# Optimization experiments

Hardware: AMD Instinct MI355X
Metric: run time of the kernel (lower is better)

The kernel has to match this reference:

```python
import jax, jax.numpy as jnp
import numpy as np

EPS = 1e-5      # BatchNorm eps
SLOPE = 0.2     # LeakyReLU negative slope
K = 20          # hardcoded k in Net
OUT_CH = 64     # AGConv out_channels
IN_CH = 6       # AGConv in_channels (= 2*3)


def _bn(x, gamma, beta, axis):
    # Inference-mode BatchNorm: running_mean=0, running_var=1
    shape = [1] * x.ndim
    shape[axis] = -1
    scale = (gamma / jnp.sqrt(1.0 + EPS)).reshape(shape)
    return x * scale + beta.reshape(shape)


def _lrelu(x):
    return jnp.where(x >= 0, x, SLOPE * x)


def _graph_feature(x, k):
    # x: (B, C, N) -> feature (B, 2C, N, k) as in get_graph_feature
    B, C, N = x.shape
    xt = jnp.swapaxes(x, 1, 2)                        # (B, N, C)
    inner = -2.0 * jnp.einsum('bci,bcj->bij', x, x)   # (B, N, N)
    xx = jnp.sum(x * x, axis=1)                       # (B, N)
    pd = -xx[:, :, None] - inner - xx[:, None, :]     # -||xi-xj||^2
    idx = jax.lax.top_k(pd, k)[1]                     # (B, N, k) nearest neighbors
    b_idx = jnp.arange(B)[:, None, None]
    nbr = xt[b_idx, idx]                              # (B, N, k, C) gather
    center = jnp.broadcast_to(xt[:, :, None, :], nbr.shape)
    feat = jnp.concatenate([nbr - center, center], axis=-1)  # (B, N, k, 2C)
    return jnp.moveaxis(feat, -1, 1)                  # (B, 2C, N, k)


def setup_inputs() -> dict:
    key = jax.random.key(0)
    ks = jax.random.split(key, 5)
    B, N = 4, 4096
    x = jax.random.normal(ks[0], (B, 3, N), dtype=jnp.float32)
    w0 = jax.random.normal(ks[1], (OUT_CH, IN_CH), dtype=jnp.float32) * 0.2
    w1 = jax.random.normal(ks[2], (OUT_CH * IN_CH, OUT_CH), dtype=jnp.float32) * 0.05
    w_out = jax.random.normal(ks[3], (3, OUT_CH), dtype=jnp.float32) * 0.1
    return {
        'x': x,
        'w0': w0, 'g0': jnp.ones(OUT_CH), 'b0': jnp.zeros(OUT_CH),
        'w1': w1, 'g1': jnp.ones(OUT_CH), 'b1': jnp.zeros(OUT_CH),
        'w_out': w_out, 'g_out': jnp.ones(3), 'b_out': jnp.zeros(3),
    }


def reference(x, w0, g0, b0, w1, g1, b1, w_out, g_out, b_out):
    # x: (B, 3, N). feat == both `x` and `p` in the torch code (points is x,
    # same idx), so compute once.
    feat = _graph_feature(x, K)                       # (B, 6, N, k)
    B, _, N, k = feat.shape
    # AGConv: weight-generating branch
    y = jnp.einsum('oc,bcnk->bonk', w0, feat)         # conv0 1x1
    y = _lrelu(_bn(y, g0, b0, 1))
    y = jnp.einsum('oc,bcnk->bonk', w1, y)            # conv1 1x1 -> (B, 384, N, k)
    y = jnp.moveaxis(y, 1, -1).reshape(B, N, k, OUT_CH, IN_CH)
    xg = jnp.moveaxis(feat, 1, -1)                    # (B, N, k, 6)
    z = jnp.einsum('bnkoc,bnkc->bnko', y, xg)         # per-edge dynamic matmul
    z = jnp.moveaxis(z, -1, 1)                        # (B, 64, N, k)
    z = _lrelu(_bn(z, g1, b1, 1))
    x1 = jnp.max(z, axis=-1)                          # max over neighbors -> (B, 64, N)
    out = jnp.einsum('oc,bcn->bon', w_out, x1)        # Net.conv1 1x1
    out = _lrelu(_bn(out, g_out, b_out, 1))
    return out
```

## Files before the change

kernel.cpp:

```cpp
#include <hip/hip_runtime.h>
#include <hip/hip_bf16.h>

#define NPTS 4096
#define BATCH 4
#define KNN 20

typedef __attribute__((ext_vector_type(8))) short bf16x8;
typedef __attribute__((ext_vector_type(4))) float f32x4;
typedef __attribute__((ext_vector_type(4))) int i32x4;
typedef unsigned long long u64;

#define OFF_W0S   0
#define OFF_B0F   384
#define OFF_S1F   448
#define OFF_B1F   512
#define OFF_WOUTS 576
#define OFF_BOUTF 768
#define OFF_WHI_BYTES 4096
#define OFF_WLO_BYTES 53248
#define OFF_IDX_BYTES 102400
#define OFF_XQ_BYTES  757760

__device__ __forceinline__ u64 shflx64(u64 v, int off) {
  int lo = __shfl_xor((int)(v & 0xFFFFFFFFull), off);
  int hi = __shfl_xor((int)(v >> 32), off);
  return ((u64)(unsigned)hi << 32) | (unsigned)lo;
}
__device__ __forceinline__ u64 shflbc64(u64 v, int src) {
  int lo = __shfl((int)(v & 0xFFFFFFFFull), src);
  int hi = __shfl((int)(v >> 32), src);
  return ((u64)(unsigned)hi << 32) | (unsigned)lo;
}

__global__ __launch_bounds__(256) void prep_kernel(
    const float* __restrict__ x,
    const float* __restrict__ w0, const float* __restrict__ g0, const float* __restrict__ b0,
    const float* __restrict__ w1, const float* __restrict__ g1, const float* __restrict__ b1,
    const float* __restrict__ wout, const float* __restrict__ gout, const float* __restrict__ bout,
    float* __restrict__ wsf, unsigned short* __restrict__ whi, unsigned short* __restrict__ wlo,
    float4* __restrict__ xq) {
  const float rs = 1.0f / sqrtf(1.0f + 1e-5f);
  int t = blockIdx.x * 256 + threadIdx.x;
  if (t < 384) wsf[OFF_W0S + t] = w0[t] * (g0[t / 6] * rs);
  if (t < 64) {
    wsf[OFF_B0F + t] = b0[t];
    wsf[OFF_S1F + t] = g1[t] * rs;
    wsf[OFF_B1F + t] = b1[t];
  }
  if (t < 192) wsf[OFF_WOUTS + t] = wout[t] * (gout[t / 64] * rs);
  if (t < 3) wsf[OFF_BOUTF + t] = bout[t];
  if (t < BATCH * NPTS) {
    int bb = t >> 12, j = t & (NPTS - 1);
    const float* xb = x + bb * 3 * NPTS;
    float x0 = xb[j], x1 = xb[NPTS + j], x2 = xb[2 * NPTS + j];
    float xx = x0 * x0 + x1 * x1 + x2 * x2;
    xq[t] = make_float4(x0, x1, x2, xx);
  }
  if (t < 24576) {
    int j = t & 7, L = (t >> 3) & 63, ft = t >> 9;
    int kk = ft >> 2, nt = ft & 3;
    int k = kk * 32 + ((L >> 4) << 3) + j;
    int c = k >> 6, d = k & 63;
    int o = nt * 16 + (L & 15);
    float w = w1[(o * 6 + c) * 64 + d];
    unsigned bw = __float_as_uint(w);
    unsigned hb = bw & 0xFFFF0000u;
    float r = w - __uint_as_float(hb);
    whi[t] = (unsigned short)(bw >> 16);
    wlo[t] = (unsigned short)(__float_as_uint(r) >> 16);
  }
}

__global__ __launch_bounds__(64, 4) void knn_kernel(const float4* __restrict__ xq,
                                                    unsigned short* __restrict__ idxbuf) {
  const int pt = blockIdx.x;
  const int b = pt >> 12, n = pt & (NPTS - 1);
  const int lane = threadIdx.x;
  const float4* xqb = xq + b * NPTS;
  const float4 xin = xqb[n];
  const float xi0 = xin.x, xi1 = xin.y, xi2 = xin.z;
  const float nxxi = -xin.w;

  u64 k1 = 0, k2 = 0;
  unsigned lo = 4095u - (unsigned)lane;
#pragma unroll 4
  for (int s = 0; s < 64; ++s) {
    float4 q = xqb[s * 64 + lane];
    float dot = xi0 * q.x + xi1 * q.y + xi2 * q.z;
    float inner = -2.0f * dot;
    float pd = (nxxi - inner) - q.w;
    u64 k = ((u64)(~__float_as_uint(pd)) << 32) | lo;
    lo -= 64u;
    bool c1 = k > k1;
    bool c2 = k > k2;
    u64 t = c1 ? k1 : k;
    k2 = c2 ? t : k2;
    k1 = c1 ? k : k1;
  }

  u64 tk = 0;
  unsigned myout = 0;
#pragma unroll 1
  for (int r = 0; r < KNN; ++r) {
    u64 bk = k1;
    for (int off = 32; off > 0; off >>= 1) {
      u64 ok = shflx64(bk, off);
      if (ok > bk) bk = ok;
    }
    unsigned bj = 4095u - (unsigned)(bk & 4095u);
    if (lane == r) myout = bj;
    bool owner = (k1 == bk);
    u64 bit = 1ull << (bj >> 6);
    if (owner) {
      tk |= bit;
      k1 = k2;
      k2 = 0;
    }
    bool need = owner && (k1 == 0);
    u64 nm = __ballot(need);
    if (nm) {
      int LN = __ffsll(nm) - 1;
      int j2 = lane * 64 + LN;
      float4 q = xqb[j2];
      float dot = xi0 * q.x + xi1 * q.y + xi2 * q.z;
      float inner = -2.0f * dot;
      float pd = (nxxi - inner) - q.w;
      u64 kk = ((u64)(~__float_as_uint(pd)) << 32) | (4095u - (unsigned)j2);
      u64 tkl = shflbc64(tk, LN);
      if ((tkl >> lane) & 1) kk = 0;
      u64 w1k = kk;
      for (int off = 32; off > 0; off >>= 1) {
        u64 ok = shflx64(w1k, off);
        if (ok > w1k) w1k = ok;
      }
      u64 kk2 = (kk == w1k) ? 0 : kk;
      u64 w2k = kk2;
      for (int off = 32; off > 0; off >>= 1) {
        u64 ok = shflx64(w2k, off);
        if (ok > w2k) w2k = ok;
      }
      if (lane == LN) { k1 = w1k; k2 = w2k; }
    }
  }
  if (lane < KNN) idxbuf[pt * KNN + lane] = (unsigned short)myout;
}

__global__ __launch_bounds__(64, 2) void mlp_kernel(const float4* __restrict__ xq,
                                                    const float* __restrict__ wsf,
                                                    const unsigned short* __restrict__ whi,
                                                    const unsigned short* __restrict__ wlo,
                                                    const unsigned short* __restrict__ idxbuf,
                                                    float* __restrict__ out) {
  __shared__ float w0l[448];
  __shared__ float v6l[80 * 12];
  __shared__ float pmax[20 * 66];

  const int lane = threadIdx.x;
  const int quad = lane >> 4, l15 = lane & 15;
  const int pt_base = blockIdx.x * 4;

  for (int i = lane; i < 448; i += 64) w0l[i] = wsf[i];

#pragma unroll
  for (int rep = 0; rep < 2; ++rep) {
    int e = rep * 64 + lane;
    if (e < 80) {
      int p = e / 20, el = e - p * 20;
      int pt = pt_base + p;
      int b = pt >> 12, n = pt & (NPTS - 1);
      float4 xi = xq[b * NPTS + n];
      int jn = idxbuf[pt * KNN + el];
      float4 xj = xq[b * NPTS + jn];
      v6l[e * 12 + 0] = xj.x - xi.x;
      v6l[e * 12 + 1] = xj.y - xi.y;
      v6l[e * 12 + 2] = xj.z - xi.z;
      v6l[e * 12 + 3] = xi.x;
      v6l[e * 12 + 4] = xi.y;
      v6l[e * 12 + 5] = xi.z;
    }
  }
  __syncthreads();

  float v6r[5][6];
#pragma unroll
  for (int t = 0; t < 5; ++t) {
    const float* vr = v6l + (t * 16 + l15) * 12;
    f32x4 a4 = *(const f32x4*)vr;
    v6r[t][0] = a4.x; v6r[t][1] = a4.y; v6r[t][2] = a4.z; v6r[t][3] = a4.w;
    v6r[t][4] = vr[4]; v6r[t][5] = vr[5];
  }
  float hf[5][2][8];
#pragma unroll
  for (int hh = 0; hh < 2; ++hh) {
#pragma unroll
    for (int j = 0; j < 8; ++j) {
      const int d = hh * 32 + quad * 8 + j;
      const float* wr = w0l + d * 6;
      float wc0 = wr[0], wc1 = wr[1], wc2 = wr[2];
      float wc3 = wr[3], wc4 = wr[4], wc5 = wr[5];
      float bb = w0l[384 + d];
#pragma unroll
      for (int t = 0; t < 5; ++t) {
        float a = bb + wc0 * v6r[t][0] + wc1 * v6r[t][1] + wc2 * v6r[t][2]
                     + wc3 * v6r[t][3] + wc4 * v6r[t][4] + wc5 * v6r[t][5];
        hf[t][hh][j] = fmaxf(a, 0.2f * a);
      }
    }
  }

  f32x4 acc[5][4];
#pragma unroll
  for (int t = 0; t < 5; ++t)
#pragma unroll
    for (int nt = 0; nt < 4; ++nt) acc[t][nt] = (f32x4){0.f, 0.f, 0.f, 0.f};

  const i32x4* whp = (const i32x4*)whi;
  const i32x4* wlp = (const i32x4*)wlo;

#pragma unroll
  for (int kk = 0; kk < 12; ++kk) {
    const int c = kk >> 1, hh = kk & 1;
    i32x4 wh[4], wl[4];
#pragma unroll
    for (int nt = 0; nt < 4; ++nt) {
      wh[nt] = whp[(kk * 4 + nt) * 64 + lane];
      wl[nt] = wlp[(kk * 4 + nt) * 64 + lane];
    }
#pragma unroll
    for (int t = 0; t < 5; ++t) {
      float vc = v6l[(t * 16 + l15) * 12 + c];
      float u0 = vc * hf[t][hh][0], u1 = vc * hf[t][hh][1];
      float u2 = vc * hf[t][hh][2], u3 = vc * hf[t][hh][3];
      float u4 = vc * hf[t][hh][4], u5 = vc * hf[t][hh][5];
      float u6 = vc * hf[t][hh][6], u7 = vc * hf[t][hh][7];
      unsigned ub0 = __float_as_uint(u0), ub1 = __float_as_uint(u1);
      unsigned ub2 = __float_as_uint(u2), ub3 = __float_as_uint(u3);
      unsigned ub4 = __float_as_uint(u4), ub5 = __float_as_uint(u5);
      unsigned ub6 = __float_as_uint(u6), ub7 = __float_as_uint(u7);
      float r0 = u0 - __uint_as_float(ub0 & 0xFFFF0000u);
      float r1 = u1 - __uint_as_float(ub1 & 0xFFFF0000u);
      float r2 = u2 - __uint_as_float(ub2 & 0xFFFF0000u);
      float r3 = u3 - __uint_as_float(ub3 & 0xFFFF0000u);
      float r4 = u4 - __uint_as_float(ub4 & 0xFFFF0000u);
      float r5 = u5 - __uint_as_float(ub5 & 0xFFFF0000u);
      float r6 = u6 - __uint_as_float(ub6 & 0xFFFF0000u);
      float r7 = u7 - __uint_as_float(ub7 & 0xFFFF0000u);
      i32x4 ah, al;
      ah.x = __builtin_amdgcn_perm(ub1, ub0, 0x07060302);
      ah.y = __builtin_amdgcn_perm(ub3, ub2, 0x07060302);
      ah.z = __builtin_amdgcn_perm(ub5, ub4, 0x07060302);
      ah.w = __builtin_amdgcn_perm(ub7, ub6, 0x07060302);
      al.x = __builtin_amdgcn_perm(__float_as_uint(r1), __float_as_uint(r0), 0x07060302);
      al.y = __builtin_amdgcn_perm(__float_as_uint(r3), __float_as_uint(r2), 0x07060302);
      al.z = __builtin_amdgcn_perm(__float_as_uint(r5), __float_as_uint(r4), 0x07060302);
      al.w = __builtin_amdgcn_perm(__float_as_uint(r7), __float_as_uint(r6), 0x07060302);
      bf16x8 ahv = __builtin_bit_cast(bf16x8, ah);
      bf16x8 alv = __builtin_bit_cast(bf16x8, al);
#pragma unroll
      for (int nt = 0; nt < 4; ++nt) {
        bf16x8 bh = __builtin_bit_cast(bf16x8, wh[nt]);
        bf16x8 bl = __builtin_bit_cast(bf16x8, wl[nt]);
        acc[t][nt] = __builtin_amdgcn_mfma_f32_16x16x32_bf16(ahv, bh, acc[t][nt], 0, 0, 0);
        acc[t][nt] = __builtin_amdgcn_mfma_f32_16x16x32_bf16(ahv, bl, acc[t][nt], 0, 0, 0);
        acc[t][nt] = __builtin_amdgcn_mfma_f32_16x16x32_bf16(alv, bh, acc[t][nt], 0, 0, 0);
      }
    }
  }
  __syncthreads();

  float s1v[4], b1v[4];
#pragma unroll
  for (int nt = 0; nt < 4; ++nt) {
    s1v[nt] = wsf[OFF_S1F + nt * 16 + l15];
    b1v[nt] = wsf[OFF_B1F + nt * 16 + l15];
  }
#pragma unroll
  for (int t = 0; t < 5; ++t) {
#pragma unroll
    for (int nt = 0; nt < 4; ++nt) {
      f32x4 a = acc[t][nt];
      float z0 = a.x * s1v[nt] + b1v[nt]; z0 = fmaxf(z0, 0.2f * z0);
      float z1 = a.y * s1v[nt] + b1v[nt]; z1 = fmaxf(z1, 0.2f * z1);
      float z2 = a.z * s1v[nt] + b1v[nt]; z2 = fmaxf(z2, 0.2f * z2);
      float z3 = a.w * s1v[nt] + b1v[nt]; z3 = fmaxf(z3, 0.2f * z3);
      float m4 = fmaxf(fmaxf(z0, z1), fmaxf(z2, z3));
      pmax[(t * 4 + quad) * 66 + nt * 16 + l15] = m4;
    }
  }
  __syncthreads();

  float woutr[3];
#pragma unroll
  for (int m = 0; m < 3; ++m) woutr[m] = wsf[OFF_WOUTS + m * 64 + lane];
#pragma unroll
  for (int p = 0; p < 4; ++p) {
    float x1 = pmax[(p * 5 + 0) * 66 + lane];
    x1 = fmaxf(x1, pmax[(p * 5 + 1) * 66 + lane]);
    x1 = fmaxf(x1, pmax[(p * 5 + 2) * 66 + lane]);
    x1 = fmaxf(x1, pmax[(p * 5 + 3) * 66 + lane]);
    x1 = fmaxf(x1, pmax[(p * 5 + 4) * 66 + lane]);
    int pt = pt_base + p;
    int b = pt >> 12, n = pt & (NPTS - 1);
#pragma unroll
    for (int m = 0; m < 3; ++m) {
      float part = woutr[m] * x1;
      for (int off = 32; off > 0; off >>= 1) part += __shfl_xor(part, off);
      if (lane == 0) {
        float ov = part + wsf[OFF_BOUTF + m];
        out[(b * 3 + m) * NPTS + n] = fmaxf(ov, 0.2f * ov);
      }
    }
  }
}

extern "C" void kernel_launch(void* const* d_in, const int* in_sizes, int n_in,
                              void* d_out, int out_size, void* d_ws, size_t ws_size,
                              hipStream_t stream) {
  const float* x    = (const float*)d_in[0];
  const float* w0   = (const float*)d_in[1];
  const float* g0   = (const float*)d_in[2];
  const float* b0   = (const float*)d_in[3];
  const float* w1   = (const float*)d_in[4];
  const float* g1   = (const float*)d_in[5];
  const float* b1   = (const float*)d_in[6];
  const float* wout = (const float*)d_in[7];
  const float* gout = (const float*)d_in[8];
  const float* bout = (const float*)d_in[9];
  float* wsf = (float*)d_ws;
  unsigned short* whi = (unsigned short*)((char*)d_ws + OFF_WHI_BYTES);
  unsigned short* wlo = (unsigned short*)((char*)d_ws + OFF_WLO_BYTES);
  unsigned short* idxbuf = (unsigned short*)((char*)d_ws + OFF_IDX_BYTES);
  float4* xq = (float4*)((char*)d_ws + OFF_XQ_BYTES);
  float* out = (float*)d_out;

  prep_kernel<<<96, 256, 0, stream>>>(x, w0, g0, b0, w1, g1, b1, wout, gout, bout,
                                      wsf, whi, wlo, xq);
  knn_kernel<<<BATCH * NPTS, 64, 0, stream>>>(xq, idxbuf);
  mlp_kernel<<<BATCH * NPTS / 4, 64, 0, stream>>>(xq, wsf, whi, wlo, idxbuf, out);
}
```

Before: 208.0 us.

## Software-pipeline MLP weight loads and split hidden features by half to cut registers

Restructures the MFMA loop in mlp_kernel into non-unrolled hh/cc loops. Each step's weight fragments are prefetched from global memory one iteration ahead into double-buffered registers. Only half of the hidden activations (hf[5][8]) are computed at a time, and v6r is reloaded per half. This is meant to hide global load latency and lower register pressure, at the cost of recomputing the v6 loads and less compiler freedom from the unroll 1 loops.

```diff
diff --git a/kernel.cpp b/kernel.cpp
--- a/kernel.cpp
+++ b/kernel.cpp
@@ -159,6 +159,16 @@
   const int quad = lane >> 4, l15 = lane & 15;
   const int pt_base = blockIdx.x * 4;
 
+  const i32x4* whp = (const i32x4*)whi;
+  const i32x4* wlp = (const i32x4*)wlo;
+
+  i32x4 wh[4], wl[4];
+#pragma unroll
+  for (int nt = 0; nt < 4; ++nt) {
+    wh[nt] = whp[nt * 64 + lane];
+    wl[nt] = wlp[nt * 64 + lane];
+  }
+
   for (int i = lane; i < 448; i += 64) w0l[i] = wsf[i];
 
 #pragma unroll
@@ -181,17 +191,23 @@
   }
   __syncthreads();
 
-  float v6r[5][6];
-#pragma unroll
-  for (int t = 0; t < 5; ++t) {
-    const float* vr = v6l + (t * 16 + l15) * 12;
-    f32x4 a4 = *(const f32x4*)vr;
-    v6r[t][0] = a4.x; v6r[t][1] = a4.y; v6r[t][2] = a4.z; v6r[t][3] = a4.w;
-    v6r[t][4] = vr[4]; v6r[t][5] = vr[5];
-  }
-  float hf[5][2][8];
-#pragma unroll
+  f32x4 acc[5][4];
+#pragma unroll
+  for (int t = 0; t < 5; ++t)
+#pragma unroll
+    for (int nt = 0; nt < 4; ++nt) acc[t][nt] = (f32x4){0.f, 0.f, 0.f, 0.f};
+
+#pragma unroll 1
   for (int hh = 0; hh < 2; ++hh) {
+    float v6r[5][6];
+#pragma unroll
+    for (int t = 0; t < 5; ++t) {
+      const float* vr = v6l + (t * 16 + l15) * 12;
+      f32x4 a4 = *(const f32x4*)vr;
+      v6r[t][0] = a4.x; v6r[t][1] = a4.y; v6r[t][2] = a4.z; v6r[t][3] = a4.w;
+      v6r[t][4] = vr[4]; v6r[t][5] = vr[5];
+    }
+    float hf[5][8];
 #pragma unroll
     for (int j = 0; j < 8; ++j) {
       const int d = hh * 32 + quad * 8 + j;
@@ -203,66 +219,65 @@
       for (int t = 0; t < 5; ++t) {
         float a = bb + wc0 * v6r[t][0] + wc1 * v6r[t][1] + wc2 * v6r[t][2]
                      + wc3 * v6r[t][3] + wc4 * v6r[t][4] + wc5 * v6r[t][5];
-        hf[t][hh][j] = fmaxf(a, 0.2f * a);
-      }
-    }
-  }
-
-  f32x4 acc[5][4];
-#pragma unroll
-  for (int t = 0; t < 5; ++t)
-#pragma unroll
-    for (int nt = 0; nt < 4; ++nt) acc[t][nt] = (f32x4){0.f, 0.f, 0.f, 0.f};
-
-  const i32x4* whp = (const i32x4*)whi;
-  const i32x4* wlp = (const i32x4*)wlo;
-
-#pragma unroll
-  for (int kk = 0; kk < 12; ++kk) {
-    const int c = kk >> 1, hh = kk & 1;
-    i32x4 wh[4], wl[4];
-#pragma unroll
-    for (int nt = 0; nt < 4; ++nt) {
-      wh[nt] = whp[(kk * 4 + nt) * 64 + lane];
-      wl[nt] = wlp[(kk * 4 + nt) * 64 + lane];
-    }
-#pragma unroll
-    for (int t = 0; t < 5; ++t) {
-      float vc = v6l[(t * 16 + l15) * 12 + c];
-      float u0 = vc * hf[t][hh][0], u1 = vc * hf[t][hh][1];
-      float u2 = vc * hf[t][hh][2], u3 = vc * hf[t][hh][3];
-      float u4 = vc * hf[t][hh][4], u5 = vc * hf[t][hh][5];
-      float u6 = vc * hf[t][hh][6], u7 = vc * hf[t][hh][7];
-      unsigned ub0 = __float_as_uint(u0), ub1 = __float_as_uint(u1);
-      unsigned ub2 = __float_as_uint(u2), ub3 = __float_as_uint(u3);
-      unsigned ub4 = __float_as_uint(u4), ub5 = __float_as_uint(u5);
-      unsigned ub6 = __float_as_uint(u6), ub7 = __float_as_uint(u7);
-      float r0 = u0 - __uint_as_float(ub0 & 0xFFFF0000u);
-      float r1 = u1 - __uint_as_float(ub1 & 0xFFFF0000u);
-      float r2 = u2 - __uint_as_float(ub2 & 0xFFFF0000u);
-      float r3 = u3 - __uint_as_float(ub3 & 0xFFFF0000u);
-      float r4 = u4 - __uint_as_float(ub4 & 0xFFFF0000u);
-      float r5 = u5 - __uint_as_float(ub5 & 0xFFFF0000u);
-      float r6 = u6 - __uint_as_float(ub6 & 0xFFFF0000u);
-      float r7 = u7 - __uint_as_float(ub7 & 0xFFFF0000u);
-      i32x4 ah, al;
-      ah.x = __builtin_amdgcn_perm(ub1, ub0, 0x07060302);
-      ah.y = __builtin_amdgcn_perm(ub3, ub2, 0x07060302);
-      ah.z = __builtin_amdgcn_perm(ub5, ub4, 0x07060302);
-      ah.w = __builtin_amdgcn_perm(ub7, ub6, 0x07060302);
-      al.x = __builtin_amdgcn_perm(__float_as_uint(r1), __float_as_uint(r0), 0x07060302);
-      al.y = __builtin_amdgcn_perm(__float_as_uint(r3), __float_as_uint(r2), 0x07060302);
-      al.z = __builtin_amdgcn_perm(__float_as_uint(r5), __float_as_uint(r4), 0x07060302);
-      al.w = __builtin_amdgcn_perm(__float_as_uint(r7), __float_as_uint(r6), 0x07060302);
-      bf16x8 ahv = __builtin_bit_cast(bf16x8, ah);
-      bf16x8 alv = __builtin_bit_cast(bf16x8, al);
-#pragma unroll
-      for (int nt = 0; nt < 4; ++nt) {
-        bf16x8 bh = __builtin_bit_cast(bf16x8, wh[nt]);
-        bf16x8 bl = __builtin_bit_cast(bf16x8, wl[nt]);
-        acc[t][nt] = __builtin_amdgcn_mfma_f32_16x16x32_bf16(ahv, bh, acc[t][nt], 0, 0, 0);
-        acc[t][nt] = __builtin_amdgcn_mfma_f32_16x16x32_bf16(ahv, bl, acc[t][nt], 0, 0, 0);
-        acc[t][nt] = __builtin_amdgcn_mfma_f32_16x16x32_bf16(alv, bh, acc[t][nt], 0, 0, 0);
+        hf[t][j] = fmaxf(a, 0.2f * a);
+      }
+    }
+
+#pragma unroll 1
+    for (int cc = 0; cc < 6; ++cc) {
+      const int kk = cc * 2 + hh;
+      const bool hasnext = !(hh == 1 && cc == 5);
+      const int kkn = (cc < 5) ? kk + 2 : 1;
+      i32x4 whn[4], wln[4];
+      if (hasnext) {
+#pragma unroll
+        for (int nt = 0; nt < 4; ++nt) {
+          whn[nt] = whp[(kkn * 4 + nt) * 64 + lane];
+          wln[nt] = wlp[(kkn * 4 + nt) * 64 + lane];
+        }
+      }
+#pragma unroll
+      for (int t = 0; t < 5; ++t) {
+        float vc = v6l[(t * 16 + l15) * 12 + cc];
+        float u0 = vc * hf[t][0], u1 = vc * hf[t][1];
+        float u2 = vc * hf[t][2], u3 = vc * hf[t][3];
+        float u4 = vc * hf[t][4], u5 = vc * hf[t][5];
+        float u6 = vc * hf[t][6], u7 = vc * hf[t][7];
+        unsigned ub0 = __float_as_uint(u0), ub1 = __float_as_uint(u1);
+        unsigned ub2 = __float_as_uint(u2), ub3 = __float_as_uint(u3);
+        unsigned ub4 = __float_as_uint(u4), ub5 = __float_as_uint(u5);
+        unsigned ub6 = __float_as_uint(u6), ub7 = __float_as_uint(u7);
+        float r0 = u0 - __uint_as_float(ub0 & 0xFFFF0000u);
+        float r1 = u1 - __uint_as_float(ub1 & 0xFFFF0000u);
+        float r2 = u2 - __uint_as_float(ub2 & 0xFFFF0000u);
+        float r3 = u3 - __uint_as_float(ub3 & 0xFFFF0000u);
+        float r4 = u4 - __uint_as_float(ub4 & 0xFFFF0000u);
+        float r5 = u5 - __uint_as_float(ub5 & 0xFFFF0000u);
+        float r6 = u6 - __uint_as_float(ub6 & 0xFFFF0000u);
+        float r7 = u7 - __uint_as_float(ub7 & 0xFFFF0000u);
+        i32x4 ah, al;
+        ah.x = __builtin_amdgcn_perm(ub1, ub0, 0x07060302);
+        ah.y = __builtin_amdgcn_perm(ub3, ub2, 0x07060302);
+        ah.z = __builtin_amdgcn_perm(ub5, ub4, 0x07060302);
+        ah.w = __builtin_amdgcn_perm(ub7, ub6, 0x07060302);
+        al.x = __builtin_amdgcn_perm(__float_as_uint(r1), __float_as_uint(r0), 0x07060302);
+        al.y = __builtin_amdgcn_perm(__float_as_uint(r3), __float_as_uint(r2), 0x07060302);
+        al.z = __builtin_amdgcn_perm(__float_as_uint(r5), __float_as_uint(r4), 0x07060302);
+        al.w = __builtin_amdgcn_perm(__float_as_uint(r7), __float_as_uint(r6), 0x07060302);
+        bf16x8 ahv = __builtin_bit_cast(bf16x8, ah);
+        bf16x8 alv = __builtin_bit_cast(bf16x8, al);
+#pragma unroll
+        for (int nt = 0; nt < 4; ++nt) {
+          bf16x8 bh = __builtin_bit_cast(bf16x8, wh[nt]);
+          bf16x8 bl = __builtin_bit_cast(bf16x8, wl[nt]);
+          acc[t][nt] = __builtin_amdgcn_mfma_f32_16x16x32_bf16(ahv, bh, acc[t][nt], 0, 0, 0);
+          acc[t][nt] = __builtin_amdgcn_mfma_f32_16x16x32_bf16(ahv, bl, acc[t][nt], 0, 0, 0);
+          acc[t][nt] = __builtin_amdgcn_mfma_f32_16x16x32_bf16(alv, bh, acc[t][nt], 0, 0, 0);
+        }
+      }
+      if (hasnext) {
+#pragma unroll
+        for (int nt = 0; nt < 4; ++nt) { wh[nt] = whn[nt]; wl[nt] = wln[nt]; }
       }
     }
   }
```

After: 189.0 us. -9.2%, faster.
